# Kernel optimization log

Hardware: AMD Instinct MI355X
Metric: run time of the kernel (lower is better)

The kernel has to match this reference:

```python
import jax, jax.numpy as jnp
import numpy as np

IN_CH, OUT_CH, MINI = 1024, 1024, 8
GY, GX = OUT_CH // MINI, IN_CH // MINI  # 128, 128
BATCH = 32768


def setup_inputs() -> dict:
    key = jax.random.key(0)
    k1, k2 = jax.random.split(key)
    x = jax.random.normal(k1, (BATCH, IN_CH), dtype=jnp.float32)
    # kaiming-style init scale for the eigens parameter
    eigens = jax.random.normal(k2, (GY, GX, MINI), dtype=jnp.float32) * (2.0 / (GX * MINI)) ** 0.5
    return {"x": x, "eigens": eigens}


def reference(x, eigens):
    # Block-circulant linear: for each (y, x_blk) grid cell, circularly convolve
    # the length-MINI eigen vector with the corresponding input block, then sum
    # over input blocks. Done in the frequency domain (full FFT, matching
    # torch.rfft(..., onesided=False) + complex_mult + irfft in the original),
    # but with the redundant gridDim_y repeat fused into a complex einsum.
    gy, gx, k = eigens.shape
    xb = x.reshape(-1, gx, k)                      # [B, GX, K]
    f_e = jnp.fft.fft(eigens, axis=-1)             # [GY, GX, K] complex
    f_x = jnp.fft.fft(xb, axis=-1)                 # [B, GX, K] complex
    f_out = jnp.einsum('yxk,bxk->byk', f_e, f_x)   # elementwise mult + sum over GX
    out = jnp.fft.ifft(f_out, axis=-1).real.astype(x.dtype)  # [B, GY, K]
    return out.reshape(-1, gy * k)                 # [B, OUT_CH]
```

## Files before the change

kernel.cpp:

```cpp
#include <hip/hip_runtime.h>
#include <stdint.h>

#define M_BATCH 32768
#define N_OUT   1024
#define K_IN    1024

#define BM 128
#define BN 128
#define BK 64
#define NT (K_IN / BK)

typedef __attribute__((ext_vector_type(8))) short  short8;
typedef __attribute__((ext_vector_type(4))) float  f32x4;

__device__ __forceinline__ unsigned short f2bf(float f) {
    __bf16 h = (__bf16)f;
    return __builtin_bit_cast(unsigned short, h);
}

typedef const __attribute__((address_space(1))) unsigned int* gas_ptr;
typedef __attribute__((address_space(3))) unsigned int*       las_ptr;

__device__ __forceinline__ void gload_lds16(const void* g, void* l) {
    __builtin_amdgcn_global_load_lds((gas_ptr)g, (las_ptr)l, 16, 0, 0);
}

__global__ __launch_bounds__(256) void build_w(const float* __restrict__ eig,
                                               unsigned short* __restrict__ W) {
    int tid = blockIdx.x * 256 + threadIdx.x;
    int y  = tid >> 7;
    int xb = tid & 127;
    const float* e = eig + (size_t)((y << 7) + xb) * 8;
    f32x4 e0 = *reinterpret_cast<const f32x4*>(e);
    f32x4 e1 = *reinterpret_cast<const f32x4*>(e + 4);
    float ev[8] = {e0[0], e0[1], e0[2], e0[3], e1[0], e1[1], e1[2], e1[3]};
#pragma unroll
    for (int j = 0; j < 8; ++j) {
        alignas(16) unsigned short wv[8];
#pragma unroll
        for (int c = 0; c < 8; ++c) wv[c] = f2bf(ev[(j - c) & 7]);
        *reinterpret_cast<uint4*>(W + (size_t)(y * 8 + j) * K_IN + xb * 8) =
            *reinterpret_cast<const uint4*>(wv);
    }
}

__global__ __launch_bounds__(256) void gemm_fused(const float* __restrict__ A,
                                                  const unsigned short* __restrict__ W,
                                                  float* __restrict__ C) {
    __shared__ unsigned short Alds[BM * BK];
    __shared__ unsigned short Blds[BN * BK];

    const int bid  = blockIdx.x;
    const int swz  = (bid & 7) * 256 + (bid >> 3);
    const int nblk = swz & 7;
    const int mblk = swz >> 3;
    const int brow = mblk * BM;
    const int bcol = nblk * BN;

    const int tid  = threadIdx.x;
    const int lane = tid & 63;
    const int wv   = tid >> 6;
    const int wm   = wv >> 1;
    const int wn   = wv & 1;

    f32x4 acc[4][4];
    const f32x4 zero = {0.f, 0.f, 0.f, 0.f};
#pragma unroll
    for (int i = 0; i < 4; ++i)
#pragma unroll
        for (int j = 0; j < 4; ++j) acc[i][j] = zero;

    const int srow  = tid >> 3;
    const int sslot = tid & 7;
    const int sk8   = sslot ^ (srow & 7);
    const float*    Af    = A + (size_t)(brow + srow) * K_IN + sk8 * 8;
    unsigned short* AldsW = Alds + srow * BK + sslot * 8;

    const int lrow = lane >> 3;
    const int lchk = (lane & 7) ^ lrow;
    const unsigned short* Bbase = W + (size_t)(bcol + wv * 32 + lrow) * K_IN + lchk * 8;
    unsigned short* BldsBase = Blds + wv * 2048;

    f32x4 aPre[4][2];
#pragma unroll
    for (int it = 0; it < 4; ++it) {
        const float* s = Af + (size_t)it * 32 * K_IN;
        aPre[it][0] = *reinterpret_cast<const f32x4*>(s);
        aPre[it][1] = *reinterpret_cast<const f32x4*>(s + 4);
    }

    for (int t = 0; t < NT; ++t) {
        const int kt  = t * BK;
        const int ktn = (kt + BK) & (K_IN - 1);

        __builtin_amdgcn_s_barrier();
        __builtin_amdgcn_sched_barrier(0);

#pragma unroll
        for (int s = 0; s < 4; ++s)
            gload_lds16(Bbase + (size_t)(s * 8) * K_IN + kt, BldsBase + s * 512);
        asm volatile("" ::: "memory");

#pragma unroll
        for (int it = 0; it < 4; ++it) {
            short8 b;
#pragma unroll
            for (int i = 0; i < 4; ++i) b[i]     = (short)f2bf(aPre[it][0][i]);
#pragma unroll
            for (int i = 0; i < 4; ++i) b[i + 4] = (short)f2bf(aPre[it][1][i]);
            *reinterpret_cast<short8*>(AldsW + it * 32 * BK) = b;
        }

#pragma unroll
        for (int it = 0; it < 4; ++it) {
            const float* s = Af + (size_t)it * 32 * K_IN + ktn;
            aPre[it][0] = *reinterpret_cast<const f32x4*>(s);
            aPre[it][1] = *reinterpret_cast<const f32x4*>(s + 4);
        }

        asm volatile("s_waitcnt vmcnt(8) lgkmcnt(0)" ::: "memory");
        __builtin_amdgcn_s_barrier();
        __builtin_amdgcn_sched_barrier(0);

#pragma unroll
        for (int ks = 0; ks < 2; ++ks) {
            short8 af[4], bfr[4];
            const int cb = ks * 4 + (lane >> 4);
            const int sl = cb ^ (lane & 7);
#pragma unroll
            for (int mt = 0; mt < 4; ++mt) {
                int row = wm * 64 + mt * 16 + (lane & 15);
                af[mt] = *reinterpret_cast<const short8*>(Alds + row * BK + sl * 8);
            }
#pragma unroll
            for (int nt = 0; nt < 4; ++nt) {
                int row = wn * 64 + nt * 16 + (lane & 15);
                bfr[nt] = *reinterpret_cast<const short8*>(Blds + row * BK + sl * 8);
            }
            __builtin_amdgcn_s_setprio(1);
#pragma unroll
            for (int mt = 0; mt < 4; ++mt)
#pragma unroll
                for (int nt = 0; nt < 4; ++nt)
                    acc[mt][nt] = __builtin_amdgcn_mfma_f32_16x16x32_bf16(
                        af[mt], bfr[nt], acc[mt][nt], 0, 0, 0);
            __builtin_amdgcn_s_setprio(0);
        }
    }

#pragma unroll
    for (int mt = 0; mt < 4; ++mt) {
#pragma unroll
        for (int nt = 0; nt < 4; ++nt) {
            int col = bcol + wn * 64 + nt * 16 + (lane & 15);
#pragma unroll
            for (int r = 0; r < 4; ++r) {
                int row = brow + wm * 64 + mt * 16 + (lane >> 4) * 4 + r;
                C[(size_t)row * N_OUT + col] = acc[mt][nt][r];
            }
        }
    }
}

extern "C" void kernel_launch(void* const* d_in, const int* in_sizes, int n_in,
                              void* d_out, int out_size, void* d_ws, size_t ws_size,
                              hipStream_t stream) {
    const float* x   = (const float*)d_in[0];
    const float* eig = (const float*)d_in[1];
    float* out = (float*)d_out;

    const size_t W_ELTS = (size_t)N_OUT * K_IN;
    if (ws_size < W_ELTS * sizeof(unsigned short)) return;
    unsigned short* W = (unsigned short*)d_ws;

    hipLaunchKernelGGL(build_w, dim3(64), dim3(256), 0, stream, eig, W);
    hipLaunchKernelGGL(gemm_fused, dim3((M_BATCH / BM) * (N_OUT / BN)), dim3(256),
                       0, stream, x, W, out);
}
```

Before: 335.1 us.

## Load A fragments directly from global into registers, dropping A LDS staging

Removes the shared-memory staging of the fp32 input tile. Each wave now loads its MFMA A fragments directly from global memory and converts them to bf16 in registers. This saves LDS space and LDS writes and reads, and adds an occupancy hint. In exchange, A is fetched redundantly by the two waves that share the same rows, and the previous software prefetch of the next A tile is lost, exposing global load latency.

```diff
diff --git a/kernel.cpp b/kernel.cpp
--- a/kernel.cpp
+++ b/kernel.cpp
@@ -44,10 +44,9 @@
     }
 }
 
-__global__ __launch_bounds__(256) void gemm_fused(const float* __restrict__ A,
-                                                  const unsigned short* __restrict__ W,
-                                                  float* __restrict__ C) {
-    __shared__ unsigned short Alds[BM * BK];
+__global__ __launch_bounds__(256, 2) void gemm_direct(const float* __restrict__ A,
+                                                      const unsigned short* __restrict__ W,
+                                                      float* __restrict__ C) {
     __shared__ unsigned short Blds[BN * BK];
 
     const int bid  = blockIdx.x;
@@ -70,81 +69,59 @@
 #pragma unroll
         for (int j = 0; j < 4; ++j) acc[i][j] = zero;
 
-    const int srow  = tid >> 3;
-    const int sslot = tid & 7;
-    const int sk8   = sslot ^ (srow & 7);
-    const float*    Af    = A + (size_t)(brow + srow) * K_IN + sk8 * 8;
-    unsigned short* AldsW = Alds + srow * BK + sslot * 8;
-
     const int lrow = lane >> 3;
     const int lchk = (lane & 7) ^ lrow;
     const unsigned short* Bbase = W + (size_t)(bcol + wv * 32 + lrow) * K_IN + lchk * 8;
     unsigned short* BldsBase = Blds + wv * 2048;
 
-    f32x4 aPre[4][2];
-#pragma unroll
-    for (int it = 0; it < 4; ++it) {
-        const float* s = Af + (size_t)it * 32 * K_IN;
-        aPre[it][0] = *reinterpret_cast<const f32x4*>(s);
-        aPre[it][1] = *reinterpret_cast<const f32x4*>(s + 4);
-    }
+    const float* Abase = A + (size_t)(brow + wm * 64 + (lane & 15)) * K_IN
+                           + (lane >> 4) * 8;
 
     for (int t = 0; t < NT; ++t) {
-        const int kt  = t * BK;
-        const int ktn = (kt + BK) & (K_IN - 1);
+        const int kt = t * BK;
 
-        __builtin_amdgcn_s_barrier();
-        __builtin_amdgcn_sched_barrier(0);
+        __syncthreads();
 
 #pragma unroll
         for (int s = 0; s < 4; ++s)
             gload_lds16(Bbase + (size_t)(s * 8) * K_IN + kt, BldsBase + s * 512);
-        asm volatile("" ::: "memory");
 
+        f32x4 aR[4][2][2];
 #pragma unroll
-        for (int it = 0; it < 4; ++it) {
-            short8 b;
+        for (int mt = 0; mt < 4; ++mt)
 #pragma unroll
-            for (int i = 0; i < 4; ++i) b[i]     = (short)f2bf(aPre[it][0][i]);
-#pragma unroll
-            for (int i = 0; i < 4; ++i) b[i + 4] = (short)f2bf(aPre[it][1][i]);
-            *reinterpret_cast<short8*>(AldsW + it * 32 * BK) = b;
-        }
+            for (int ks = 0; ks < 2; ++ks) {
+                const float* s = Abase + (size_t)(mt * 16) * K_IN + kt + ks * 32;
+                aR[mt][ks][0] = *reinterpret_cast<const f32x4*>(s);
+                aR[mt][ks][1] = *reinterpret_cast<const f32x4*>(s + 4);
+            }
 
-#pragma unroll
-        for (int it = 0; it < 4; ++it) {
-            const float* s = Af + (size_t)it * 32 * K_IN + ktn;
-            aPre[it][0] = *reinterpret_cast<const f32x4*>(s);
-            aPre[it][1] = *reinterpret_cast<const f32x4*>(s + 4);
-        }
-
-        asm volatile("s_waitcnt vmcnt(8) lgkmcnt(0)" ::: "memory");
-        __builtin_amdgcn_s_barrier();
-        __builtin_amdgcn_sched_barrier(0);
+        __syncthreads();
 
 #pragma unroll
         for (int ks = 0; ks < 2; ++ks) {
-            short8 af[4], bfr[4];
+            short8 af[4];
+#pragma unroll
+            for (int mt = 0; mt < 4; ++mt) {
+#pragma unroll
+                for (int i = 0; i < 4; ++i) af[mt][i]     = (short)f2bf(aR[mt][ks][0][i]);
+#pragma unroll
+                for (int i = 0; i < 4; ++i) af[mt][i + 4] = (short)f2bf(aR[mt][ks][1][i]);
+            }
+            short8 bfr[4];
             const int cb = ks * 4 + (lane >> 4);
             const int sl = cb ^ (lane & 7);
-#pragma unroll
-            for (int mt = 0; mt < 4; ++mt) {
-                int row = wm * 64 + mt * 16 + (lane & 15);
-                af[mt] = *reinterpret_cast<const short8*>(Alds + row * BK + sl * 8);
-            }
 #pragma unroll
             for (int nt = 0; nt < 4; ++nt) {
                 int row = wn * 64 + nt * 16 + (lane & 15);
                 bfr[nt] = *reinterpret_cast<const short8*>(Blds + row * BK + sl * 8);
             }
-            __builtin_amdgcn_s_setprio(1);
 #pragma unroll
             for (int mt = 0; mt < 4; ++mt)
 #pragma unroll
                 for (int nt = 0; nt < 4; ++nt)
                     acc[mt][nt] = __builtin_amdgcn_mfma_f32_16x16x32_bf16(
                         af[mt], bfr[nt], acc[mt][nt], 0, 0, 0);
-            __builtin_amdgcn_s_setprio(0);
         }
     }
 
@@ -174,6 +151,6 @@
     unsigned short* W = (unsigned short*)d_ws;
 
     hipLaunchKernelGGL(build_w, dim3(64), dim3(256), 0, stream, eig, W);
-    hipLaunchKernelGGL(gemm_fused, dim3((M_BATCH / BM) * (N_OUT / BN)), dim3(256),
+    hipLaunchKernelGGL(gemm_direct, dim3((M_BATCH / BM) * (N_OUT / BN)), dim3(256),
                        0, stream, x, W, out);
 }
```

Result: slower. 432.4 us (+29.0%).
